# Optimization experiments

Measured on AMD Instinct MI355X. Metric: run time of the kernel, lower is better.

Reference implementation:

```python
import jax, jax.numpy as jnp
import numpy as np
from jax import lax

K = 3          # kernel_size
G = 8          # group count in SIFA
EPS = 1e-5     # BN and GN eps


def _bn(x, g, b, m, v):
    # eval-mode BatchNorm2d over channel dim 1
    scale = (g / jnp.sqrt(v + EPS))[None, :, None, None]
    shift = (b - m * g / jnp.sqrt(v + EPS))[None, :, None, None]
    return x * scale + shift


def setup_inputs() -> dict:
    key = jax.random.key(0)
    ks = jax.random.split(key, 20)
    B, C, H, W, OUP = 8, 64, 128, 128, 128
    CE = C * K * K  # expanded channels = 576
    CG = C // G     # channels per group view = 8
    f32 = jnp.float32
    inp = {
        "x": jax.random.normal(ks[0], (B, C, H, W), f32),
        # depthwise generate conv: groups=C, out=C*K^2 -> OIHW [CE,1,K,K]
        "gen_w": jax.random.normal(ks[1], (CE, 1, K, K), f32) * 0.1,
        "gen_bn_g": jnp.ones((CE,), f32) + 0.1 * jax.random.normal(ks[2], (CE,), f32),
        "gen_bn_b": 0.1 * jax.random.normal(ks[3], (CE,), f32),
        "gen_bn_m": 0.05 * jax.random.normal(ks[4], (CE,), f32),
        "gen_bn_v": jax.random.uniform(ks[5], (CE,), f32, 0.5, 1.5),
        # GroupNorm(num_groups=CG, num_channels=CG) affine params
        "gn_w": jnp.ones((CG,), f32) + 0.1 * jax.random.normal(ks[6], (CG,), f32),
        "gn_b": 0.1 * jax.random.normal(ks[7], (CG,), f32),
        # gating params, shape (1, CG, 1, 1)
        "cweight": 0.1 * jax.random.normal(ks[8], (1, CG, 1, 1), f32),
        "cbias": jnp.ones((1, CG, 1, 1), f32) + 0.1 * jax.random.normal(ks[9], (1, CG, 1, 1), f32),
        "sweight": 0.1 * jax.random.normal(ks[10], (1, CG, 1, 1), f32),
        "sbias": jnp.ones((1, CG, 1, 1), f32) + 0.1 * jax.random.normal(ks[11], (1, CG, 1, 1), f32),
        "weights_add": jnp.asarray(0.5, f32),
        # final Conv: C -> OUP, k=K, s=K, p=0, bias=False + BN + SiLU
        "conv_w": jax.random.normal(ks[12], (OUP, C, K, K), f32) * (1.0 / np.sqrt(C * K * K)),
        "conv_bn_g": jnp.ones((OUP,), f32) + 0.1 * jax.random.normal(ks[13], (OUP,), f32),
        "conv_bn_b": 0.1 * jax.random.normal(ks[14], (OUP,), f32),
        "conv_bn_m": 0.05 * jax.random.normal(ks[15], (OUP,), f32),
        "conv_bn_v": jax.random.uniform(ks[16], (OUP,), f32, 0.5, 1.5),
    }
    return inp


def reference(x, gen_w, gen_bn_g, gen_bn_b, gen_bn_m, gen_bn_v,
              gn_w, gn_b, cweight, cbias, sweight, sbias, weights_add,
              conv_w, conv_bn_g, conv_bn_b, conv_bn_m, conv_bn_v):
    B, C, H, W = x.shape
    # --- generate: depthwise conv (groups=C) + BN + ReLU ---
    y = lax.conv_general_dilated(
        x, gen_w, window_strides=(1, 1), padding=[(K // 2, K // 2)] * 2,
        feature_group_count=C,
        dimension_numbers=("NCHW", "OIHW", "NCHW"))  # [B, C*K*K, H, W]
    y = jax.nn.relu(_bn(y, gen_bn_g, gen_bn_b, gen_bn_m, gen_bn_v))
    # --- rearrange 'b c (n1 n2) h w -> b c (h n1) (w n2)' ---
    y = y.reshape(B, C, K, K, H, W)          # (b, c, n1, n2, h, w)
    y = y.transpose(0, 1, 4, 2, 5, 3)        # (b, c, h, n1, w, n2)
    HK, WK = H * K, W * K
    y = y.reshape(B, C, HK, WK)
    # --- group view: (b*G, C//G, HK, WK) ---
    g = y.reshape(B * G, C // G, HK, WK)
    # channel gate: global avg pool -> affine -> sigmoid
    x_ch = jnp.mean(g, axis=(2, 3), keepdims=True)        # [B*G, CG, 1, 1]
    ch = g * jax.nn.sigmoid(cweight * x_ch + cbias)
    # spatial gate: per-channel GroupNorm (num_groups == num_channels)
    mu = jnp.mean(g, axis=(2, 3), keepdims=True)
    var = jnp.var(g, axis=(2, 3), keepdims=True)
    gnorm = (g - mu) / jnp.sqrt(var + EPS)
    gnorm = gnorm * gn_w[None, :, None, None] + gn_b[None, :, None, None]
    sp = g * jax.nn.sigmoid(sweight * gnorm + sbias)
    out = weights_add * ch + (1.0 - weights_add) * sp
    out = out.reshape(B, C, HK, WK)
    # --- final Conv: k=K, s=K, p=0, no bias + BN + SiLU ---
    z = lax.conv_general_dilated(
        out, conv_w, window_strides=(K, K), padding="VALID",
        dimension_numbers=("NCHW", "OIHW", "NCHW"))       # [B, OUP, H, W]
    z = _bn(z, conv_bn_g, conv_bn_b, conv_bn_m, conv_bn_v)
    return z * jax.nn.sigmoid(z)  # SiLU
```

## Files before the change

### kernel.cpp

```cpp
#include <hip/hip_runtime.h>
#include <math.h>


#define EPSF 1e-5f
typedef _Float16 v8h __attribute__((ext_vector_type(8)));
typedef __fp16 fp16x2 __attribute__((ext_vector_type(2)));
typedef float v4f __attribute__((ext_vector_type(4)));

static constexpr int C_ = 64, HW_ = 16384, W_ = 128;

static constexpr int WS_WFOLD = 0;
static constexpr int WS_SHIFT = 5184;
static constexpr int WS_BIAS  = 5760;
static constexpr int WS_GATE  = 5888;
static constexpr int WS_PART  = 7936;
static constexpr int WS_WH    = 12032;

__device__ __forceinline__ float sigmf(float v) { return 1.f / (1.f + __expf(-v)); }

__global__ __launch_bounds__(256) void k_fold(
    const float* __restrict__ gen_w,
    const float* __restrict__ gg, const float* __restrict__ gb,
    const float* __restrict__ gm, const float* __restrict__ gv,
    const float* __restrict__ conv_w,
    const float* __restrict__ cg, const float* __restrict__ cb,
    const float* __restrict__ cm, const float* __restrict__ cv,
    float* __restrict__ ws)
{
    int idx = blockIdx.x * 256 + threadIdx.x;
    _Float16* Whp = (_Float16*)(ws + WS_WH);
    if (idx < 131072) {
        int oup = idx >> 10, kk = idx & 1023, c = kk >> 4, j = kk & 15;
        float s = cg[oup] * rsqrtf(cv[oup] + EPSF);
        float v = (j < 9) ? conv_w[(oup * C_ + c) * 9 + j] * s : 0.f;
        Whp[idx] = (_Float16)v;
    } else if (idx < 136256) {
        int i = idx - 131072; int ce = i / 9;
        float s = gg[ce] * rsqrtf(gv[ce] + EPSF);
        ws[WS_WFOLD + i] = gen_w[i] * s;
    } else if (idx < 136832) {
        int ce = idx - 136256;
        float s = gg[ce] * rsqrtf(gv[ce] + EPSF);
        ws[WS_SHIFT + ce] = gb[ce] - gm[ce] * s;
    } else if (idx < 136960) {
        int oup = idx - 136832;
        float s = cg[oup] * rsqrtf(cv[oup] + EPSF);
        ws[WS_BIAS + oup] = cb[oup] - cm[oup] * s;
    }
}

__global__ __launch_bounds__(256) void k_stats(
    const float* __restrict__ x, const float* __restrict__ ws,
    float* __restrict__ part)
{
    __shared__ float xs[34 * 132];
    __shared__ __align__(16) float wfl[84];
    __shared__ float shl[9];
    __shared__ float r1[256], r2[256];
    int bid = blockIdx.x; int b = bid >> 8; int c = (bid >> 2) & 63; int q = bid & 3;
    int t = threadIdx.x;
    const float* xp = x + (size_t)(b * C_ + c) * HW_;
    for (int i = t; i < 4420; i += 256) {
        int r = i / 130, cc = i - r * 130;
        int yy = q * 32 + r - 1, xx = cc - 1;
        float v = 0.f;
        if (yy >= 0 && yy < 128 && xx >= 0 && xx < 128) v = xp[yy * 128 + xx];
        xs[r * 132 + cc] = v;
    }
    if (t < 84) wfl[t] = ws[WS_WFOLD + c * 81 + ((t < 81) ? t : 80)];
    if (t >= 84 && t < 93) shl[t - 84] = ws[WS_SHIFT + c * 9 + (t - 84)];
    __syncthreads();

    float wv[84];
#pragma unroll
    for (int i = 0; i < 21; ++i) *(float4*)&wv[i * 4] = *(const float4*)&wfl[i * 4];
    float sh9[9];
#pragma unroll
    for (int i = 0; i < 9; ++i) sh9[i] = shl[i];

    float s1 = 0.f, s2 = 0.f;
    for (int i = 0; i < 16; ++i) {
        int id = i * 256 + t; int row = id >> 7, col = id & 127;
        float nb[9];
#pragma unroll
        for (int dy = 0; dy < 3; ++dy)
#pragma unroll
            for (int dx = 0; dx < 3; ++dx) nb[dy * 3 + dx] = xs[(row + dy) * 132 + col + dx];
        float uv[9];
#pragma unroll
        for (int j = 0; j < 9; ++j) uv[j] = sh9[j];
#pragma unroll
        for (int k = 0; k < 9; ++k) {
            float xv = nb[k];
#pragma unroll
            for (int j = 0; j < 9; ++j) uv[j] = fmaf(wv[j * 9 + k], xv, uv[j]);
        }
#pragma unroll
        for (int j = 0; j < 9; ++j) {
            float v = fmaxf(uv[j], 0.f);
            s1 += v; s2 = fmaf(v, v, s2);
        }
    }
    r1[t] = s1; r2[t] = s2;
    __syncthreads();
    for (int s = 128; s > 0; s >>= 1) {
        if (t < s) { r1[t] += r1[t + s]; r2[t] += r2[t + s]; }
        __syncthreads();
    }
    if (t == 0) { part[bid * 2] = r1[0]; part[bid * 2 + 1] = r2[0]; }
}

__global__ __launch_bounds__(256) void k_gate(
    const float* __restrict__ part,
    const float* __restrict__ cwt, const float* __restrict__ cbs,
    const float* __restrict__ swt, const float* __restrict__ sbs,
    const float* __restrict__ gnw, const float* __restrict__ gnb,
    const float* __restrict__ wadd, float4* __restrict__ gate)
{
    int i = blockIdx.x * 256 + threadIdx.x;
    if (i >= 512) return;
    int b = i >> 6, c = i & 63;
    float s1 = 0.f, s2 = 0.f;
    for (int q = 0; q < 4; ++q) {
        int pi = (b * 256 + c * 4 + q) * 2;
        s1 += part[pi]; s2 += part[pi + 1];
    }
    const float N = 9.f * 16384.f;
    float mean = s1 / N;
    float var = s2 / N - mean * mean;
    float inv = rsqrtf(var + EPSF);
    int cgi = c & 7;
    float wa = wadd[0];
    float cgt = sigmf(cwt[cgi] * mean + cbs[cgi]);
    const float NL2E = -1.44269504f;
    float4 o;
    o.x = wa * cgt;
    o.y = 1.f - wa;
    o.z = NL2E * (swt[cgi] * gnw[cgi] * inv);
    o.w = NL2E * (swt[cgi] * (gnb[cgi] - mean * inv * gnw[cgi]) + sbs[cgi]);
    gate[i] = o;
}

__global__ __launch_bounds__(256) void k_main(
    const float* __restrict__ x, const float* __restrict__ ws,
    float* __restrict__ out)
{
    __shared__ _Float16 u_s[128 * 64];
    __shared__ _Float16 W_s[128 * 64];
    __shared__ float xs[2][4 * 200];
    __shared__ float bias_s[128];

    int t = threadIdx.x;
    int bid = blockIdx.x;
    int b = bid >> 7, tile = bid & 127;
    int oh0 = (tile >> 3) << 3;
    int ow0 = (tile & 7) << 4;
    if (t < 128) bias_s[t] = ws[WS_BIAS + t];

    const float* xb = x + (size_t)b * C_ * HW_;
    const _Float16* Wh = (const _Float16*)(ws + WS_WH);

    int w = __builtin_amdgcn_readfirstlane(t >> 6);
    int lane = t & 63, quad = lane >> 4, l15 = lane & 15;
    int col = lane & 15, prow0 = (lane >> 4) << 1;

    v4f acc[4][4];
#pragma unroll
    for (int a = 0; a < 4; ++a)
#pragma unroll
        for (int bb = 0; bb < 4; ++bb) acc[a][bb] = (v4f)0.f;

    {
        const float* xc = xb + (size_t)w * HW_;
#pragma unroll
        for (int i = 0; i < 3; ++i) {
            int item = lane + i * 64;
            if (item < 180) {
                int r = item / 18, cl = item - r * 18;
                int yy = oh0 + r - 1, xx = ow0 + cl - 1;
                float v = 0.f;
                if (yy >= 0 && yy < 128 && xx >= 0 && xx < 128) v = xc[yy * 128 + xx];
                xs[0][w * 200 + r * 20 + cl] = v;
            }
        }
    }
    __syncthreads();

    int buf = 0;
    for (int it = 0; it < 16; ++it) {
        int c = it * 4 + w;

        float4 wld[4];
#pragma unroll
        for (int i = 0; i < 4; ++i) {
            int id = t + i * 256; int oup = id >> 3, kb = id & 7;
            wld[i] = *(const float4*)(Wh + oup * 1024 + it * 64 + kb * 8);
        }

        const float* xw = &xs[buf][w * 200];
        float nb[12];
#pragma unroll
        for (int dr = 0; dr < 4; ++dr)
#pragma unroll
            for (int dc = 0; dc < 3; ++dc)
                nb[dr * 3 + dc] = xw[(prow0 + dr) * 20 + col + dc];

        const float* wfp = ws + WS_WFOLD + c * 81;
        const float* shp = ws + WS_SHIFT + c * 9;
        float4 g4 = *(const float4*)(ws + WS_GATE + (((b << 6) + c) << 2));

        int p0 = prow0 * 16 + col;
        int swzA0 = ((2 * w) ^ (p0 & 7)) << 3;
        int swzA1 = ((2 * w) ^ ((p0 + 16) & 7)) << 3;
        int swzB0 = ((2 * w + 1) ^ (p0 & 7)) << 3;
        int swzB1 = ((2 * w + 1) ^ ((p0 + 16) & 7)) << 3;

#pragma unroll 1
        for (int jp = 0; jp < 4; ++jp) {
            float wl[18];
#pragma unroll
            for (int i = 0; i < 18; ++i) wl[i] = wfp[jp * 18 + i];
            float s0 = shp[jp * 2], s1v = shp[jp * 2 + 1];
#pragma unroll
            for (int px = 0; px < 2; ++px) {
                float a0 = s0, a1 = s1v;
#pragma unroll
                for (int k = 0; k < 9; ++k) {
                    float xv = nb[(px + k / 3) * 3 + (k % 3)];
                    a0 = fmaf(wl[k], xv, a0);
                    a1 = fmaf(wl[9 + k], xv, a1);
                }
                float v0 = fmaxf(a0, 0.f), v1 = fmaxf(a1, 0.f);
                float e0 = __builtin_amdgcn_exp2f(fmaf(g4.z, v0, g4.w));
                float e1 = __builtin_amdgcn_exp2f(fmaf(g4.z, v1, g4.w));
                float u0 = v0 * fmaf(g4.y, __builtin_amdgcn_rcpf(1.f + e0), g4.x);
                float u1 = v1 * fmaf(g4.y, __builtin_amdgcn_rcpf(1.f + e1), g4.x);
                int base = (p0 + px * 16) * 64 + (px ? swzA1 : swzA0);
                *(fp16x2*)&u_s[base + jp * 2] = __builtin_amdgcn_cvt_pkrtz(u0, u1);
            }
        }
        {
            float w9[9];
#pragma unroll
            for (int i = 0; i < 9; ++i) w9[i] = wfp[72 + i];
            float s8 = shp[8];
#pragma unroll
            for (int px = 0; px < 2; ++px) {
                float a0 = s8;
#pragma unroll
                for (int k = 0; k < 9; ++k)
                    a0 = fmaf(w9[k], nb[(px + k / 3) * 3 + (k % 3)], a0);
                float v0 = fmaxf(a0, 0.f);
                float e0 = __builtin_amdgcn_exp2f(fmaf(g4.z, v0, g4.w));
                float u8 = v0 * fmaf(g4.y, __builtin_amdgcn_rcpf(1.f + e0), g4.x);
                union { fp16x2 p[4]; float4 f; } z;
                z.p[0] = __builtin_amdgcn_cvt_pkrtz(u8, 0.f);
                z.p[1] = __builtin_amdgcn_cvt_pkrtz(0.f, 0.f);
                z.p[2] = z.p[1]; z.p[3] = z.p[1];
                int base = (p0 + px * 16) * 64 + (px ? swzB1 : swzB0);
                *(float4*)&u_s[base] = z.f;
            }
        }

#pragma unroll
        for (int i = 0; i < 4; ++i) {
            int id = t + i * 256; int oup = id >> 3, kb = id & 7;
            *(float4*)&W_s[oup * 64 + ((kb ^ (oup & 7)) << 3)] = wld[i];
        }
        if (it < 15) {
            const float* xc = xb + (size_t)(it * 4 + 4 + w) * HW_;
#pragma unroll
            for (int i = 0; i < 3; ++i) {
                int item = lane + i * 64;
                if (item < 180) {
                    int r = item / 18, cl = item - r * 18;
                    int yy = oh0 + r - 1, xx = ow0 + cl - 1;
                    float v = 0.f;
                    if (yy >= 0 && yy < 128 && xx >= 0 && xx < 128) v = xc[yy * 128 + xx];
                    xs[buf ^ 1][w * 200 + r * 20 + cl] = v;
                }
            }
        }
        __syncthreads();

#pragma unroll
        for (int ks = 0; ks < 2; ++ks) {
            int kb = ks * 4 + quad;
            v8h A[4], Bf[4];
#pragma unroll
            for (int a = 0; a < 4; ++a) {
                int row = ((w & 1) << 6) + (a << 4) + l15;
                A[a] = *(const v8h*)&W_s[row * 64 + ((kb ^ (row & 7)) << 3)];
            }
#pragma unroll
            for (int bb = 0; bb < 4; ++bb) {
                int row = ((w >> 1) << 6) + (bb << 4) + l15;
                Bf[bb] = *(const v8h*)&u_s[row * 64 + ((kb ^ (row & 7)) << 3)];
            }
#pragma unroll
            for (int a = 0; a < 4; ++a)
#pragma unroll
                for (int bb = 0; bb < 4; ++bb)
                    acc[a][bb] = __builtin_amdgcn_mfma_f32_16x16x32_f16(A[a], Bf[bb], acc[a][bb], 0, 0, 0);
        }
        __syncthreads();
        buf ^= 1;
    }

    size_t ob = (size_t)b * 128 * HW_;
#pragma unroll
    for (int a = 0; a < 4; ++a) {
#pragma unroll
        for (int r = 0; r < 4; ++r) {
            int oup = ((w & 1) << 6) + (a << 4) + (quad << 2) + r;
            float bo = bias_s[oup];
#pragma unroll
            for (int bb = 0; bb < 4; ++bb) {
                int p2 = ((w >> 1) << 6) + (bb << 4) + l15;
                int py2 = p2 >> 4, px2 = p2 & 15;
                float z = acc[a][bb][r] + bo;
                out[ob + (size_t)oup * HW_ + (oh0 + py2) * W_ + ow0 + px2] = z * sigmf(z);
            }
        }
    }
}

extern "C" void kernel_launch(void* const* d_in, const int* in_sizes, int n_in,
                              void* d_out, int out_size, void* d_ws, size_t ws_size,
                              hipStream_t stream)
{
    const float* x      = (const float*)d_in[0];
    const float* gen_w  = (const float*)d_in[1];
    const float* gg     = (const float*)d_in[2];
    const float* gb     = (const float*)d_in[3];
    const float* gm     = (const float*)d_in[4];
    const float* gv     = (const float*)d_in[5];
    const float* gnw    = (const float*)d_in[6];
    const float* gnb    = (const float*)d_in[7];
    const float* cwt    = (const float*)d_in[8];
    const float* cbs    = (const float*)d_in[9];
    const float* swt    = (const float*)d_in[10];
    const float* sbs    = (const float*)d_in[11];
    const float* wadd   = (const float*)d_in[12];
    const float* conv_w = (const float*)d_in[13];
    const float* cg2    = (const float*)d_in[14];
    const float* cb2    = (const float*)d_in[15];
    const float* cm2    = (const float*)d_in[16];
    const float* cv2    = (const float*)d_in[17];
    float* ws  = (float*)d_ws;
    float* out = (float*)d_out;

    k_fold<<<535, 256, 0, stream>>>(gen_w, gg, gb, gm, gv, conv_w, cg2, cb2, cm2, cv2, ws);
    k_stats<<<2048, 256, 0, stream>>>(x, ws, ws + WS_PART);
    k_gate<<<2, 256, 0, stream>>>(ws + WS_PART, cwt, cbs, swt, sbs, gnw, gnb, wadd,
                                  (float4*)(ws + WS_GATE));
    k_main<<<1024, 256, 0, stream>>>(x, ws, out);
}
```

Baseline: 252.6 us.

## Restructure stats kernel to reuse neighborhoods across rows and stream weights

The stats kernel now has each thread preload a 4x(6x3) window of input neighbors into registers and produce four consecutive rows per window. It loops over output channels in pairs, reading the folded weights straight from global (scalar/uniform) memory instead of staging 84 weights in registers via shared memory. The aim is fewer shared-memory reads per output and lower register pressure from the weight array, at the cost of more global weight loads. The fp16 store in the main kernel is also rewritten with a float vector in place of a union.

```diff
diff --git a/kernel.cpp b/kernel.cpp
--- a/kernel.cpp
+++ b/kernel.cpp
@@ -54,8 +54,6 @@
     float* __restrict__ part)
 {
     __shared__ float xs[34 * 132];
-    __shared__ __align__(16) float wfl[84];
-    __shared__ float shl[9];
     __shared__ float r1[256], r2[256];
     int bid = blockIdx.x; int b = bid >> 8; int c = (bid >> 2) & 63; int q = bid & 3;
     int t = threadIdx.x;
@@ -67,39 +65,61 @@
         if (yy >= 0 && yy < 128 && xx >= 0 && xx < 128) v = xp[yy * 128 + xx];
         xs[r * 132 + cc] = v;
     }
-    if (t < 84) wfl[t] = ws[WS_WFOLD + c * 81 + ((t < 81) ? t : 80)];
-    if (t >= 84 && t < 93) shl[t - 84] = ws[WS_SHIFT + c * 9 + (t - 84)];
     __syncthreads();
-
-    float wv[84];
-#pragma unroll
-    for (int i = 0; i < 21; ++i) *(float4*)&wv[i * 4] = *(const float4*)&wfl[i * 4];
-    float sh9[9];
-#pragma unroll
-    for (int i = 0; i < 9; ++i) sh9[i] = shl[i];
-
+    const float* wfp = ws + WS_WFOLD + c * 81;
+    const float* shp = ws + WS_SHIFT + c * 9;
+    int col = t & 127, half = t >> 7;
+
+    float nb[72];
+#pragma unroll
+    for (int i = 0; i < 4; ++i) {
+        int r0 = half * 4 + i * 8;
+#pragma unroll
+        for (int rr = 0; rr < 6; ++rr)
+#pragma unroll
+            for (int dc = 0; dc < 3; ++dc)
+                nb[i * 18 + rr * 3 + dc] = xs[(r0 + rr) * 132 + col + dc];
+    }
     float s1 = 0.f, s2 = 0.f;
-    for (int i = 0; i < 16; ++i) {
-        int id = i * 256 + t; int row = id >> 7, col = id & 127;
-        float nb[9];
-#pragma unroll
-        for (int dy = 0; dy < 3; ++dy)
-#pragma unroll
-            for (int dx = 0; dx < 3; ++dx) nb[dy * 3 + dx] = xs[(row + dy) * 132 + col + dx];
-        float uv[9];
-#pragma unroll
-        for (int j = 0; j < 9; ++j) uv[j] = sh9[j];
-#pragma unroll
-        for (int k = 0; k < 9; ++k) {
-            float xv = nb[k];
-#pragma unroll
-            for (int j = 0; j < 9; ++j) uv[j] = fmaf(wv[j * 9 + k], xv, uv[j]);
-        }
-#pragma unroll
-        for (int j = 0; j < 9; ++j) {
-            float v = fmaxf(uv[j], 0.f);
-            s1 += v; s2 = fmaf(v, v, s2);
-        }
+#pragma unroll 1
+    for (int jp = 0; jp < 4; ++jp) {
+        float wl[18];
+#pragma unroll
+        for (int i = 0; i < 18; ++i) wl[i] = wfp[jp * 18 + i];
+        float sA = shp[jp * 2], sB = shp[jp * 2 + 1];
+#pragma unroll
+        for (int i = 0; i < 4; ++i)
+#pragma unroll
+            for (int p = 0; p < 4; ++p) {
+                float a0 = sA, a1 = sB;
+#pragma unroll
+                for (int k = 0; k < 9; ++k) {
+                    float xv = nb[i * 18 + (p + k / 3) * 3 + (k % 3)];
+                    a0 = fmaf(wl[k], xv, a0);
+                    a1 = fmaf(wl[9 + k], xv, a1);
+                }
+                float v0 = fmaxf(a0, 0.f), v1 = fmaxf(a1, 0.f);
+                s1 += v0 + v1;
+                s2 = fmaf(v0, v0, s2);
+                s2 = fmaf(v1, v1, s2);
+            }
+    }
+    {
+        float wl[9];
+#pragma unroll
+        for (int i = 0; i < 9; ++i) wl[i] = wfp[72 + i];
+        float s8 = shp[8];
+#pragma unroll
+        for (int i = 0; i < 4; ++i)
+#pragma unroll
+            for (int p = 0; p < 4; ++p) {
+                float a0 = s8;
+#pragma unroll
+                for (int k = 0; k < 9; ++k)
+                    a0 = fmaf(wl[k], nb[i * 18 + (p + k / 3) * 3 + (k % 3)], a0);
+                float v0 = fmaxf(a0, 0.f);
+                s1 += v0; s2 = fmaf(v0, v0, s2);
+            }
     }
     r1[t] = s1; r2[t] = s2;
     __syncthreads();
@@ -253,12 +273,11 @@
                 float v0 = fmaxf(a0, 0.f);
                 float e0 = __builtin_amdgcn_exp2f(fmaf(g4.z, v0, g4.w));
                 float u8 = v0 * fmaf(g4.y, __builtin_amdgcn_rcpf(1.f + e0), g4.x);
-                union { fp16x2 p[4]; float4 f; } z;
-                z.p[0] = __builtin_amdgcn_cvt_pkrtz(u8, 0.f);
-                z.p[1] = __builtin_amdgcn_cvt_pkrtz(0.f, 0.f);
-                z.p[2] = z.p[1]; z.p[3] = z.p[1];
+                v4f zf;
+                zf[0] = __builtin_bit_cast(float, __builtin_amdgcn_cvt_pkrtz(u8, 0.f));
+                zf[1] = 0.f; zf[2] = 0.f; zf[3] = 0.f;
                 int base = (p0 + px * 16) * 64 + (px ? swzB1 : swzB0);
-                *(float4*)&u_s[base] = z.f;
+                *(v4f*)&u_s[base] = zf;
             }
         }
 
```

Result: slower. 260.2 us (+3.0%).
